# Kernel optimization log

Measured on AMD Instinct MI355X. Metric: run time of the kernel, lower is better.

Reference implementation:

```python
import jax, jax.numpy as jnp
import numpy as np

N = 8192
IN_F = 256
OUT_F = 64
ALPHA = 0.3  # LeakyReLU negative slope
NEG_INF = -9e15


def setup_inputs() -> dict:
    key = jax.random.key(0)
    k1, k2, k3, k4 = jax.random.split(key, 4)
    h = jax.random.normal(k1, (N, IN_F), dtype=jnp.float32)
    # sparse-ish binary adjacency with self loops (values are 0/1 floats)
    adj = (jax.random.uniform(k2, (N, N)) < 0.05).astype(jnp.float32)
    adj = jnp.maximum(adj, jnp.eye(N, dtype=jnp.float32))
    # xavier_uniform-style scales (gain=1.414)
    w_lim = 1.414 * np.sqrt(6.0 / (IN_F + OUT_F))
    a_lim = 1.414 * np.sqrt(6.0 / (2 * OUT_F + 1))
    W = jax.random.uniform(k3, (IN_F, OUT_F), minval=-w_lim, maxval=w_lim, dtype=jnp.float32)
    a = jax.random.uniform(k4, (2 * OUT_F, 1), minval=-a_lim, maxval=a_lim, dtype=jnp.float32)
    return {"h": h, "adj": adj, "W": W, "a": a}


def reference(h, adj, W, a):
    # Wh: [N, F]
    Wh = h @ W
    # Additive decomposition of the original concat-attention:
    # e_ij = leakyrelu(a[:F].Wh_i + a[F:].Wh_j)  -- identical math, no NxNx2F tensor
    src = Wh @ a[:OUT_F]      # [N, 1]
    dst = Wh @ a[OUT_F:]      # [N, 1]
    e = jax.nn.leaky_relu(src + dst.T, negative_slope=ALPHA)  # [N, N]
    e = e * adj               # faithful: original multiplies by adj before masking
    att = jnp.where(adj > 0, e, NEG_INF)
    att = jax.nn.softmax(att, axis=1)
    # dropout omitted (eval mode / deterministic reference)
    h_prime = att @ Wh        # [N, F]
    return jax.nn.elu(h_prime)
```

## Files before the change

### kernel.cpp

```cpp
#include <hip/hip_runtime.h>
#include <hip/hip_bf16.h>

#define N_NODES 8192
#define IN_F    256
#define OUT_F   64
#define ALPHA   0.3f
#define MBIAS   20.0f
#define CSPL    8
#define COLS_PER (N_NODES / CSPL)
#define NTILES  (COLS_PER / 64)
#define ROWS    32
#define LDP     72

typedef unsigned short u16;
typedef unsigned int   u32;
typedef __attribute__((ext_vector_type(8))) short bf16x8;
typedef __attribute__((ext_vector_type(4))) float f32x4;

__device__ __forceinline__ float bf2f(u32 u) { return __uint_as_float(u << 16); }
__device__ __forceinline__ u32 f2bfbits(float x) {
    u32 u = __float_as_uint(x);
    return (u + 0x7FFFu + ((u >> 16) & 1u)) >> 16;
}
__device__ __forceinline__ float lrelu(float s) { return s > 0.f ? s : ALPHA * s; }

__device__ __forceinline__ int detect_bf16(const void* adj) {
    return ((((const u32*)adj)[0] & 0xFFFFu) == 0x3F80u) ? 1 : 0;
}

template <bool BF16>
__device__ __forceinline__ float ld(const void* p, size_t idx) {
    if constexpr (BF16) return bf2f(((const u16*)p)[idx]);
    else                return ((const float*)p)[idx];
}

template <bool BF16>
__device__ __forceinline__ void wh4_impl(
    const void* __restrict__ h, const void* __restrict__ W,
    const void* __restrict__ a, float* __restrict__ src,
    float* __restrict__ dst, int i0, int lane, float* accv)
{
    float acc0 = 0.f, acc1 = 0.f, acc2 = 0.f, acc3 = 0.f;
#pragma unroll 8
    for (int k = 0; k < IN_F; ++k) {
        float wv = ld<BF16>(W, (size_t)k * OUT_F + lane);
        float h0 = ld<BF16>(h, (size_t)(i0 + 0) * IN_F + k);
        float h1 = ld<BF16>(h, (size_t)(i0 + 1) * IN_F + k);
        float h2 = ld<BF16>(h, (size_t)(i0 + 2) * IN_F + k);
        float h3 = ld<BF16>(h, (size_t)(i0 + 3) * IN_F + k);
        acc0 = fmaf(h0, wv, acc0);
        acc1 = fmaf(h1, wv, acc1);
        acc2 = fmaf(h2, wv, acc2);
        acc3 = fmaf(h3, wv, acc3);
    }
    float av = ld<BF16>(a, lane);
    float bv = ld<BF16>(a, OUT_F + lane);
    float accs[4] = {acc0, acc1, acc2, acc3};
#pragma unroll
    for (int r = 0; r < 4; ++r) {
        float ps = accs[r] * av, pd = accs[r] * bv;
#pragma unroll
        for (int off = 32; off > 0; off >>= 1) {
            ps += __shfl_xor(ps, off, 64);
            pd += __shfl_xor(pd, off, 64);
        }
        if (lane == 0) { src[i0 + r] = ps; dst[i0 + r] = pd; }
        accv[r] = accs[r];
    }
}

__global__ __launch_bounds__(256) void gat_wh_kernel(
    const void* __restrict__ h, const void* __restrict__ W,
    const void* __restrict__ a, const void* __restrict__ adj,
    u16* __restrict__ WhT, float* __restrict__ src, float* __restrict__ dst)
{
    __shared__ float accs[16][OUT_F];
    const int tid = threadIdx.x, wave = tid >> 6, lane = tid & 63;
    const int i0 = blockIdx.x * 16 + wave * 4;
    float av[4];
    if (detect_bf16(adj)) wh4_impl<true >(h, W, a, src, dst, i0, lane, av);
    else                  wh4_impl<false>(h, W, a, src, dst, i0, lane, av);
#pragma unroll
    for (int r = 0; r < 4; ++r) accs[wave * 4 + r][lane] = av[r];
    __syncthreads();
    if (tid < OUT_F) {
        u32 w[8];
#pragma unroll
        for (int e = 0; e < 8; ++e) {
            u32 lo = f2bfbits(accs[2 * e][tid]);
            u32 hi = f2bfbits(accs[2 * e + 1][tid]);
            w[e] = lo | (hi << 16);
        }
        u16* dstp = WhT + (size_t)tid * N_NODES + blockIdx.x * 16;
        *(uint4*)dstp       = *(uint4*)&w[0];
        *(uint4*)(dstp + 8) = *(uint4*)&w[4];
    }
}

__global__ __launch_bounds__(256, 8) void gat_attn_kernel(
    const void* __restrict__ adj, const u16* __restrict__ WhT,
    const float* __restrict__ src, const float* __restrict__ dst,
    float* __restrict__ O_part, float* __restrict__ l_part)
{
    __shared__ alignas(16) u16 Plds[ROWS * LDP];
    __shared__ alignas(16) u16 Blds[64 * LDP];

    const int tid = threadIdx.x, wave = tid >> 6, lane = tid & 63;
    const int r  = tid >> 3, cq = tid & 7;
    const int br = tid >> 2, bq = tid & 3;
    const int i0 = blockIdx.x * ROWS, c0 = blockIdx.y * COLS_PER;
    const int isbf = detect_bf16(adj);

    const float srow = src[i0 + r];
    const float m = lrelu(srow + MBIAS);

    const u16*    whtrow = WhT + (size_t)br * N_NODES + c0 + bq * 16;
    const float4* dstp   = (const float4*)(dst + c0 + cq * 8);
    const u16*    adj16  = (const u16*)adj   + (size_t)(i0 + r) * N_NODES + c0 + cq * 8;
    const float*  adj32  = (const float*)adj + (size_t)(i0 + r) * N_NODES + c0 + cq * 8;

    const int mw = wave & 1, nw = wave >> 1;
    const int mrow = lane & 15, kq = (lane >> 4) * 8;

    f32x4 acc[2] = {{0,0,0,0},{0,0,0,0}};
    float lacc = 0.f;

    for (int t = 0; t < NTILES; ++t) {
        uint4 b0 = *(const uint4*)(whtrow + t * 64);
        uint4 b1 = *(const uint4*)(whtrow + t * 64 + 8);
        *(uint4*)&Blds[br * LDP + bq * 16]     = b0;
        *(uint4*)&Blds[br * LDP + bq * 16 + 8] = b1;

        u32 msk = 0;
        if (isbf) {
            uint4 av = *(const uint4*)(adj16 + t * 64);
            u32 aw[4] = {av.x, av.y, av.z, av.w};
#pragma unroll
            for (int e = 0; e < 4; ++e) {
                if (aw[e] & 0xFFFFu) msk |= (1u << (2 * e));
                if (aw[e] >> 16)     msk |= (1u << (2 * e + 1));
            }
        } else {
            uint4 a0 = *(const uint4*)(adj32 + t * 64);
            uint4 a1 = *(const uint4*)(adj32 + t * 64 + 4);
            u32 aw[8] = {a0.x,a0.y,a0.z,a0.w, a1.x,a1.y,a1.z,a1.w};
#pragma unroll
            for (int e = 0; e < 8; ++e)
                if (aw[e]) msk |= (1u << e);
        }
        float4 d0 = dstp[t * 16], d1 = dstp[t * 16 + 1];
        float dv[8] = {d0.x,d0.y,d0.z,d0.w, d1.x,d1.y,d1.z,d1.w};
        u32 po[4];
#pragma unroll
        for (int e = 0; e < 4; ++e) {
            float s0 = lrelu(srow + dv[2 * e]);
            float s1 = lrelu(srow + dv[2 * e + 1]);
            float p0 = (msk & (1u << (2 * e)))     ? __expf(s0 - m) : 0.f;
            float p1 = (msk & (1u << (2 * e + 1))) ? __expf(s1 - m) : 0.f;
            u32 q0 = f2bfbits(p0), q1 = f2bfbits(p1);
            lacc += bf2f(q0) + bf2f(q1);
            po[e] = q0 | (q1 << 16);
        }
        *(uint4*)&Plds[r * LDP + cq * 8] = *(uint4*)&po[0];

        __syncthreads();

#pragma unroll
        for (int ks = 0; ks < 2; ++ks) {
            bf16x8 avf = *(bf16x8*)&Plds[(16 * mw + mrow) * LDP + ks * 32 + kq];
#pragma unroll
            for (int nt2 = 0; nt2 < 2; ++nt2) {
                int nt = nw * 2 + nt2;
                bf16x8 bvf = *(bf16x8*)&Blds[(16 * nt + mrow) * LDP + ks * 32 + kq];
                acc[nt2] = __builtin_amdgcn_mfma_f32_16x16x32_bf16(avf, bvf, acc[nt2], 0, 0, 0);
            }
        }
        __syncthreads();
    }

    lacc += __shfl_xor(lacc, 1, 64);
    lacc += __shfl_xor(lacc, 2, 64);
    lacc += __shfl_xor(lacc, 4, 64);
    if (cq == 0) l_part[blockIdx.y * N_NODES + i0 + r] = lacc;

    float* Ob = O_part + (size_t)blockIdx.y * N_NODES * OUT_F;
#pragma unroll
    for (int nt2 = 0; nt2 < 2; ++nt2) {
        int nt = nw * 2 + nt2;
#pragma unroll
        for (int reg = 0; reg < 4; ++reg) {
            int row = i0 + 16 * mw + (lane >> 4) * 4 + reg;
            int col = 16 * nt + (lane & 15);
            Ob[(size_t)row * OUT_F + col] = acc[nt2][reg];
        }
    }
}

__global__ __launch_bounds__(256) void gat_reduce_kernel(
    const float* __restrict__ O_part, const float* __restrict__ l_part,
    const void* __restrict__ adj, void* __restrict__ out)
{
    int gid = blockIdx.x * 256 + threadIdx.x;
    int i = gid >> 6;
    float O = 0.f, L = 0.f;
#pragma unroll
    for (int c = 0; c < CSPL; ++c) {
        O += O_part[(size_t)c * N_NODES * OUT_F + gid];
        L += l_part[c * N_NODES + i];
    }
    float hp = O / L;
    float o = hp > 0.f ? hp : expm1f(hp);
    if (detect_bf16(adj)) ((u16*)out)[gid] = (u16)f2bfbits(o);
    else                  ((float*)out)[gid] = o;
}

extern "C" void kernel_launch(void* const* d_in, const int* in_sizes, int n_in,
                              void* d_out, int out_size, void* d_ws, size_t ws_size,
                              hipStream_t stream)
{
    const void* h   = d_in[0];
    const void* adj = d_in[1];
    const void* W   = d_in[2];
    const void* a   = d_in[3];

    char* ws = (char*)d_ws;
    u16*   WhT    = (u16*)ws;
    float* src    = (float*)(ws + (1u << 20));
    float* dst    = (float*)(ws + (1u << 20) + 32768);
    float* O_part = (float*)(ws + (2u << 20));
    float* l_part = (float*)(ws + (18u << 20));

    gat_wh_kernel<<<N_NODES / 16, 256, 0, stream>>>(h, W, a, adj, WhT, src, dst);
    dim3 grid(N_NODES / ROWS, CSPL);
    gat_attn_kernel<<<grid, 256, 0, stream>>>(adj, WhT, src, dst, O_part, l_part);
    gat_reduce_kernel<<<N_NODES * OUT_F / 256, 256, 0, stream>>>(O_part, l_part, adj, d_out);
}
```

Before: 441.2 us.

## Precompute adjacency bitmask in a separate pass, stage per-block masks in LDS

```diff
diff --git a/kernel.cpp b/kernel.cpp
--- a/kernel.cpp
+++ b/kernel.cpp
@@ -11,9 +11,11 @@
 #define NTILES  (COLS_PER / 64)
 #define ROWS    32
 #define LDP     72
+#define MROW    136
 
 typedef unsigned short u16;
 typedef unsigned int   u32;
+typedef unsigned long long u64;
 typedef __attribute__((ext_vector_type(8))) short bf16x8;
 typedef __attribute__((ext_vector_type(4))) float f32x4;
 
@@ -32,6 +34,39 @@
 __device__ __forceinline__ float ld(const void* p, size_t idx) {
     if constexpr (BF16) return bf2f(((const u16*)p)[idx]);
     else                return ((const float*)p)[idx];
+}
+
+__global__ __launch_bounds__(256) void gat_mask_kernel(
+    const void* __restrict__ adj, u64* __restrict__ mask64)
+{
+    const int lane = threadIdx.x & 63;
+    const int wgid = blockIdx.x * 4 + (threadIdx.x >> 6);
+    const int NW   = 2048 * 4;
+    const int C    = (N_NODES / 256) * N_NODES;
+
+    if (detect_bf16(adj)) {
+        const u16* base = (const u16*)adj;
+        for (int c = wgid; c < C; c += NW) {
+            const u16* p = base + (size_t)c * 256;
+            u64 b0 = __ballot(p[lane]       != 0);
+            u64 b1 = __ballot(p[64  + lane] != 0);
+            u64 b2 = __ballot(p[128 + lane] != 0);
+            u64 b3 = __ballot(p[192 + lane] != 0);
+            u64 v = (lane == 0) ? b0 : (lane == 1) ? b1 : (lane == 2) ? b2 : b3;
+            if (lane < 4) mask64[(size_t)c * 4 + lane] = v;
+        }
+    } else {
+        const float* base = (const float*)adj;
+        for (int c = wgid; c < C; c += NW) {
+            const float* p = base + (size_t)c * 256;
+            u64 b0 = __ballot(p[lane]       != 0.f);
+            u64 b1 = __ballot(p[64  + lane] != 0.f);
+            u64 b2 = __ballot(p[128 + lane] != 0.f);
+            u64 b3 = __ballot(p[192 + lane] != 0.f);
+            u64 v = (lane == 0) ? b0 : (lane == 1) ? b1 : (lane == 2) ? b2 : b3;
+            if (lane < 4) mask64[(size_t)c * 4 + lane] = v;
+        }
+    }
 }
 
 template <bool BF16>
@@ -97,33 +132,40 @@
     }
 }
 
-__global__ __launch_bounds__(256, 8) void gat_attn_kernel(
-    const void* __restrict__ adj, const u16* __restrict__ WhT,
+__global__ __launch_bounds__(256, 4) void gat_attn_kernel(
+    const u64* __restrict__ mask64, const u16* __restrict__ WhT,
     const float* __restrict__ src, const float* __restrict__ dst,
     float* __restrict__ O_part, float* __restrict__ l_part)
 {
     __shared__ alignas(16) u16 Plds[ROWS * LDP];
     __shared__ alignas(16) u16 Blds[64 * LDP];
+    __shared__ alignas(16) unsigned char Mlds[ROWS * MROW];
 
     const int tid = threadIdx.x, wave = tid >> 6, lane = tid & 63;
     const int r  = tid >> 3, cq = tid & 7;
     const int br = tid >> 2, bq = tid & 3;
     const int i0 = blockIdx.x * ROWS, c0 = blockIdx.y * COLS_PER;
-    const int isbf = detect_bf16(adj);
+
+    {
+        const unsigned char* mb = (const unsigned char*)mask64;
+        uint4 v = *(const uint4*)(mb + (size_t)(i0 + (tid >> 3)) * (N_NODES / 8)
+                                     + (c0 >> 3) + (tid & 7) * 16);
+        *(uint4*)&Mlds[(tid >> 3) * MROW + (tid & 7) * 16] = v;
+    }
 
     const float srow = src[i0 + r];
     const float m = lrelu(srow + MBIAS);
 
     const u16*    whtrow = WhT + (size_t)br * N_NODES + c0 + bq * 16;
     const float4* dstp   = (const float4*)(dst + c0 + cq * 8);
-    const u16*    adj16  = (const u16*)adj   + (size_t)(i0 + r) * N_NODES + c0 + cq * 8;
-    const float*  adj32  = (const float*)adj + (size_t)(i0 + r) * N_NODES + c0 + cq * 8;
 
     const int mw = wave & 1, nw = wave >> 1;
     const int mrow = lane & 15, kq = (lane >> 4) * 8;
 
     f32x4 acc[2] = {{0,0,0,0},{0,0,0,0}};
     float lacc = 0.f;
+
+    __syncthreads();
 
     for (int t = 0; t < NTILES; ++t) {
         uint4 b0 = *(const uint4*)(whtrow + t * 64);
@@ -131,23 +173,7 @@
         *(uint4*)&Blds[br * LDP + bq * 16]     = b0;
         *(uint4*)&Blds[br * LDP + bq * 16 + 8] = b1;
 
-        u32 msk = 0;
-        if (isbf) {
-            uint4 av = *(const uint4*)(adj16 + t * 64);
-            u32 aw[4] = {av.x, av.y, av.z, av.w};
-#pragma unroll
-            for (int e = 0; e < 4; ++e) {
-                if (aw[e] & 0xFFFFu) msk |= (1u << (2 * e));
-                if (aw[e] >> 16)     msk |= (1u << (2 * e + 1));
-            }
-        } else {
-            uint4 a0 = *(const uint4*)(adj32 + t * 64);
-            uint4 a1 = *(const uint4*)(adj32 + t * 64 + 4);
-            u32 aw[8] = {a0.x,a0.y,a0.z,a0.w, a1.x,a1.y,a1.z,a1.w};
-#pragma unroll
-            for (int e = 0; e < 8; ++e)
-                if (aw[e]) msk |= (1u << e);
-        }
+        u32 msk = Mlds[r * MROW + t * 8 + cq];
         float4 d0 = dstp[t * 16], d1 = dstp[t * 16 + 1];
         float dv[8] = {d0.x,d0.y,d0.z,d0.w, d1.x,d1.y,d1.z,d1.w};
         u32 po[4];
@@ -227,11 +253,13 @@
     u16*   WhT    = (u16*)ws;
     float* src    = (float*)(ws + (1u << 20));
     float* dst    = (float*)(ws + (1u << 20) + 32768);
-    float* O_part = (float*)(ws + (2u << 20));
-    float* l_part = (float*)(ws + (18u << 20));
-
+    u64*   mask64 = (u64*)  (ws + (2u << 20));
+    float* O_part = (float*)(ws + (16u << 20));
+    float* l_part = (float*)(ws + (32u << 20));
+
+    gat_mask_kernel<<<2048, 256, 0, stream>>>(adj, mask64);
     gat_wh_kernel<<<N_NODES / 16, 256, 0, stream>>>(h, W, a, adj, WhT, src, dst);
     dim3 grid(N_NODES / ROWS, CSPL);
-    gat_attn_kernel<<<grid, 256, 0, stream>>>(adj, WhT, src, dst, O_part, l_part);
+    gat_attn_kernel<<<grid, 256, 0, stream>>>(mask64, WhT, src, dst, O_part, l_part);
     gat_reduce_kernel<<<N_NODES * OUT_F / 256, 256, 0, stream>>>(O_part, l_part, adj, d_out);
 }
```

Result: faster. 426.8 us (-3.2%).
